# Optimization experiments

Measured on AMD Instinct MI355X. Metric: run time of the kernel, lower is better.

## Reference

```python
import jax, jax.numpy as jnp
import numpy as np

N, E, D, G = 50000, 600000, 128, 64
EPS = 1e-5


def prelu(x, a):
    return jnp.where(x >= 0, x, a * x)


def degree_norms(edge_src, edge_dst):
    ones = jnp.ones((E,), jnp.float32)
    deg_out = jax.ops.segment_sum(ones, edge_src, num_segments=N)
    deg_in = jax.ops.segment_sum(ones, edge_dst, num_segments=N)
    norm_src = jnp.where(deg_out > 0, jax.lax.rsqrt(jnp.maximum(deg_out, 1.0)), 0.0)
    norm_dst = jnp.where(deg_in > 0, jax.lax.rsqrt(jnp.maximum(deg_in, 1.0)), 0.0)
    return norm_src, norm_dst


def graph_conv(x, W, b, alpha, edge_src, edge_dst, norm_src, norm_dst):
    # DGL GraphConv norm='both': D_out^{-1/2} on src, aggregate, D_in^{-1/2} on dst, then linear
    xs = x * norm_src[:, None]
    agg = jax.ops.segment_sum(xs[edge_src], edge_dst, num_segments=N)
    agg = agg * norm_dst[:, None]
    h = agg @ W + b
    return prelu(h, alpha)


def batch_norm(h, gamma, beta):
    mean = jnp.mean(h, axis=0)
    var = jnp.mean(jnp.square(h - mean), axis=0)
    return (h - mean) * jax.lax.rsqrt(var + EPS) * gamma + beta


def setup_inputs() -> dict:
    key = jax.random.key(0)
    ks = jax.random.split(key, 8)
    inp = {
        "heat": jax.random.normal(ks[0], (N, D), jnp.float32),
        "edge_src": jax.random.randint(ks[1], (E,), 0, N, jnp.int32),
        "edge_dst": jax.random.randint(ks[2], (E,), 0, N, jnp.int32),
        "graph_ids": jnp.sort(jax.random.randint(ks[3], (N,), 0, G, jnp.int32)),
    }
    for i in range(2):
        kw = jax.random.fold_in(ks[4], i)
        inp[f"W{i}"] = jax.random.normal(kw, (D, D), jnp.float32) * (1.0 / np.sqrt(D))
        inp[f"b{i}"] = jnp.zeros((D,), jnp.float32)
        inp[f"ac{i}"] = jnp.float32(0.25)  # conv PReLU alpha
        inp[f"g{i}"] = jnp.ones((D,), jnp.float32)
        inp[f"be{i}"] = jnp.zeros((D,), jnp.float32)
        inp[f"aa{i}"] = jnp.float32(0.25)  # outer PReLU alpha
    return inp


def reference(heat, edge_src, edge_dst, graph_ids,
              W0, b0, ac0, g0, be0, aa0,
              W1, b1, ac1, g1, be1, aa1):
    norm_src, norm_dst = degree_norms(edge_src, edge_dst)
    x = heat  # dropout in eval mode -> identity
    h = graph_conv(x, W0, b0, ac0, edge_src, edge_dst, norm_src, norm_dst)
    h = prelu(batch_norm(h, g0, be0), aa0)
    gh = jax.ops.segment_sum(h, graph_ids, num_segments=G)
    h = graph_conv(h, W1, b1, ac1, edge_src, edge_dst, norm_src, norm_dst)
    h = prelu(batch_norm(h, g1, be1), aa1)
    gh = gh + jax.ops.segment_sum(h, graph_ids, num_segments=G)
    return h, gh
```

## Files before the change

### kernel.cpp

```cpp
#include <hip/hip_runtime.h>
#include <hip/hip_fp8.h>

#define NN 50000
#define NE 600000
#define DD 128
#define GG 64
#define EPS 1e-5f
#define CAP 64
#define HB 60
#define ECHUNK 10000
#define HALF 25000
#define HWORDS 12500
#define ZROW 50000
#define NBUILD ((NE + 255) / 256)
#define NPB (NN * 16 / 256)

typedef unsigned short u16;
typedef unsigned int u32;
typedef unsigned char u8;
typedef u16 u16x8 __attribute__((ext_vector_type(8)));
typedef u8 u8x16 __attribute__((ext_vector_type(16)));
typedef u8 u8x8 __attribute__((ext_vector_type(8)));
typedef short bf16x8 __attribute__((ext_vector_type(8)));
typedef float f32x4 __attribute__((ext_vector_type(4)));

__device__ __forceinline__ float bf2f(u16 v) {
    return __uint_as_float(((u32)v) << 16);
}
__device__ __forceinline__ u16 f2bf(float f) {
    u32 u = __float_as_uint(f);
    u += 0x7fff + ((u >> 16) & 1);
    return (u16)(u >> 16);
}
__device__ __forceinline__ float f8tof(u8 b) {
    __hip_fp8_e4m3 v;
    v.__x = b;
    return (float)v;
}
__device__ __forceinline__ u8 ftof8(float f) {
    return __hip_fp8_e4m3(f).__x;
}

__global__ void k_wprep(const float* __restrict__ W0, const float* __restrict__ W1,
                        u16* __restrict__ wtb, int* __restrict__ cnt_in,
                        float* __restrict__ stats , float* __restrict__ gh,
                        u8* __restrict__ xsb) {
    int k = threadIdx.x;
    int c = blockIdx.x;
    int lay = blockIdx.y;
    const float* W = lay ? W1 : W0;
    wtb[lay * DD * DD + c * DD + k] = f2bf(W[k * DD + c]);

    int gtid = (blockIdx.y * gridDim.x + blockIdx.x) * DD + threadIdx.x;
    for (int i = gtid; i < NN; i += 32768) cnt_in[i] = 0;
    if (gtid < 4 * DD) stats[gtid] = 0.f;
    if (gtid < GG * DD) gh[gtid] = 0.f;
    if (gtid < 16) {
        u8x8 z = {0, 0, 0, 0, 0, 0, 0, 0};
        *(u8x8*)(xsb + (size_t)ZROW * DD + gtid * 8) = z;
    }
}

__global__ __launch_bounds__(256) void k_prep(
        const int* __restrict__ src, const int* __restrict__ dst,
        u32* __restrict__ partials, int* __restrict__ cnt_in, u16* __restrict__ csr) {
    __shared__ u32 hc[HWORDS];
    int blk = blockIdx.x;
    int t = threadIdx.x;
    if (blk >= 2 * HB) {
        int e = (blk - 2 * HB) * 256 + t;
        if (e < NE) {
            int d = dst[e];
            int pos = atomicAdd(&cnt_in[d], 1);
            if (pos < CAP) csr[(size_t)d * CAP + pos] = (u16)src[e];
        }
        return;
    }
    int b = blk % HB, p = blk / HB;
    for (int i = t; i < HWORDS; i += 256) hc[i] = 0;
    __syncthreads();
    int lo = p * HALF;
    int e0 = b * ECHUNK;
    for (int e = e0 + t; e < e0 + ECHUNK; e += 256) {
        int s = src[e] - lo;
        if ((u32)s < (u32)HALF) atomicAdd(&hc[s >> 1], 1u << ((s & 1) << 4));
    }
    __syncthreads();
    u32* outp = partials + (size_t)(p * HB + b) * HWORDS;
    for (int i = t; i < HWORDS; i += 256) outp[i] = hc[i];
}

__global__ void k_hist_reduce(const u32* __restrict__ partials, const int* __restrict__ cnt_in,
                              float* __restrict__ norm_src, float* __restrict__ norm_dst) {
    int j = blockIdx.x * 256 + threadIdx.x;
    int p = blockIdx.y;
    if (j < HWORDS) {
        u32 s = 0;
#pragma unroll 4
        for (int b = 0; b < HB; ++b) s += partials[(size_t)(p * HB + b) * HWORDS + j];
        int n0 = p * HALF + 2 * j;
        u32 c0 = s & 0xffffu, c1 = s >> 16;
        norm_src[n0]     = c0 ? rsqrtf((float)c0) : 0.f;
        norm_src[n0 + 1] = c1 ? rsqrtf((float)c1) : 0.f;
        int d0 = cnt_in[n0], d1 = cnt_in[n0 + 1];
        norm_dst[n0]     = d0 > 0 ? rsqrtf((float)d0) : 0.f;
        norm_dst[n0 + 1] = d1 > 0 ? rsqrtf((float)d1) : 0.f;
    }
}

__global__ void k_scale_rows(const float* __restrict__ norm_src, const float* __restrict__ x,
                             u8* __restrict__ xsb) {
    int idx = blockIdx.x * 256 + threadIdx.x;
    int row = idx >> 4;
    int c8 = (idx & 15) << 3;
    float ns = norm_src[row];
    const float4* xp = (const float4*)(x + (size_t)row * DD + c8);
    float4 a = xp[0], b = xp[1];
    u8x8 o;
    o[0] = ftof8(a.x * ns); o[1] = ftof8(a.y * ns); o[2] = ftof8(a.z * ns); o[3] = ftof8(a.w * ns);
    o[4] = ftof8(b.x * ns); o[5] = ftof8(b.y * ns); o[6] = ftof8(b.z * ns); o[7] = ftof8(b.w * ns);
    *(u8x8*)(xsb + (size_t)row * DD + c8) = o;
}

#define LOADF8(v, ii)                                                    \
    u8x16 v##0 = *(const u8x16*)(xcol + (size_t)(ii)[0] * DD);           \
    u8x16 v##1 = *(const u8x16*)(xcol + (size_t)(ii)[1] * DD);           \
    u8x16 v##2 = *(const u8x16*)(xcol + (size_t)(ii)[2] * DD);           \
    u8x16 v##3 = *(const u8x16*)(xcol + (size_t)(ii)[3] * DD);           \
    u8x16 v##4 = *(const u8x16*)(xcol + (size_t)(ii)[4] * DD);           \
    u8x16 v##5 = *(const u8x16*)(xcol + (size_t)(ii)[5] * DD);           \
    u8x16 v##6 = *(const u8x16*)(xcol + (size_t)(ii)[6] * DD);           \
    u8x16 v##7 = *(const u8x16*)(xcol + (size_t)(ii)[7] * DD);

#define ACCF8(acc, v)                                                    \
    _Pragma("unroll")                                                    \
    for (int j = 0; j < 16; ++j) {                                       \
        float a01 = f8tof(v##0[j]) + f8tof(v##1[j]);                     \
        float a23 = f8tof(v##2[j]) + f8tof(v##3[j]);                     \
        float a45 = f8tof(v##4[j]) + f8tof(v##5[j]);                     \
        float a67 = f8tof(v##6[j]) + f8tof(v##7[j]);                     \
        acc[j] += (a01 + a23) + (a45 + a67);                             \
    }

__global__ __launch_bounds__(256) void k_gg(
        const u8* __restrict__ xsb, const int* __restrict__ cnt_in,
        const u16* __restrict__ csr, const float* __restrict__ norm_dst,
        const u16* __restrict__ wtb, const float* __restrict__ bias,
        const float* __restrict__ ac, u16* __restrict__ hpreb,
        float* __restrict__ sums, float* __restrict__ sumsq) {
    __shared__ u16 sAg[4][16][DD + 8];
    __shared__ float sStat[2][4][DD];
    int t = threadIdx.x;
    int w = t >> 6;
    int l = t & 63;
    int rb = blockIdx.x * 64 + w * 16;
    bool wvalid = (rb < NN);
    int cl8 = l & 7;
    int rw = l >> 3;
    const u8* xcol = xsb + cl8 * 16;

    if (wvalid) {
#pragma unroll
        for (int gp = 0; gp < 2; ++gp) {
            int r = rb + gp * 8 + rw;
            int cnt = min(cnt_in[r], CAP);
            const u16* ce = csr + (size_t)r * CAP;
            float acc[16];
#pragma unroll
            for (int j = 0; j < 16; ++j) acc[j] = 0.f;
            int e = 0;
            for (; e + 8 <= cnt; e += 8) {
                u16x8 ii = *(const u16x8*)(ce + e);
                LOADF8(va, ii)
                ACCF8(acc, va)
            }
            if (e < cnt) {
                u16x8 ii = *(const u16x8*)(ce + e);
                int jj[8];
#pragma unroll
                for (int j = 0; j < 8; ++j) jj[j] = (e + j < cnt) ? (int)ii[j] : ZROW;
                LOADF8(vm, jj)
                ACCF8(acc, vm)
            }
            float nd = norm_dst[r];
            u16x8 o0, o1;
#pragma unroll
            for (int j = 0; j < 8; ++j) {
                o0[j] = f2bf(acc[j] * nd);
                o1[j] = f2bf(acc[8 + j] * nd);
            }
            *(u16x8*)&sAg[w][gp * 8 + rw][cl8 * 16] = o0;
            *(u16x8*)&sAg[w][gp * 8 + rw][cl8 * 16 + 8] = o1;
        }
    }
    __syncthreads();

    int lr = l & 15;
    int kg = l >> 4;
    float alpha = ac[0];

    bf16x8 afrag[4];
    if (wvalid) {
        const u16* abase = &sAg[w][lr][kg * 8];
        afrag[0] = *(const bf16x8*)(abase);
        afrag[1] = *(const bf16x8*)(abase + 32);
        afrag[2] = *(const bf16x8*)(abase + 64);
        afrag[3] = *(const bf16x8*)(abase + 96);
    }

#pragma unroll
    for (int ct = 0; ct < 8; ++ct) {
        int c = ct * 16;
        float sS = 0.f, sQ = 0.f;
        if (wvalid) {
            const u16* bbase = wtb + (size_t)(c + lr) * DD + kg * 8;
            bf16x8 b0 = *(const bf16x8*)(bbase);
            bf16x8 b1 = *(const bf16x8*)(bbase + 32);
            bf16x8 b2 = *(const bf16x8*)(bbase + 64);
            bf16x8 b3 = *(const bf16x8*)(bbase + 96);
            float bv = bias[c + lr];
            f32x4 acc = {bv, bv, bv, bv};
            acc = __builtin_amdgcn_mfma_f32_16x16x32_bf16(afrag[0], b0, acc, 0, 0, 0);
            acc = __builtin_amdgcn_mfma_f32_16x16x32_bf16(afrag[1], b1, acc, 0, 0, 0);
            acc = __builtin_amdgcn_mfma_f32_16x16x32_bf16(afrag[2], b2, acc, 0, 0, 0);
            acc = __builtin_amdgcn_mfma_f32_16x16x32_bf16(afrag[3], b3, acc, 0, 0, 0);
#pragma unroll
            for (int j = 0; j < 4; ++j) {
                float h = acc[j];
                h = h >= 0.f ? h : alpha * h;
                u16 hb = f2bf(h);
                float hq = bf2f(hb);
                int grow = rb + kg * 4 + j;
                hpreb[(size_t)grow * DD + c + lr] = hb;
                sS += hq;
                sQ += hq * hq;
            }
        }
        sS += __shfl_xor(sS, 16); sS += __shfl_xor(sS, 32);
        sQ += __shfl_xor(sQ, 16); sQ += __shfl_xor(sQ, 32);
        if (kg == 0) {
            sStat[0][w][c + lr] = sS;
            sStat[1][w][c + lr] = sQ;
        }
    }
    __syncthreads();
    if (t < DD) {
        float s = sStat[0][0][t] + sStat[0][1][t] + sStat[0][2][t] + sStat[0][3][t];
        atomicAdd(&sums[t], s);
    } else if (t < 2 * DD) {
        int c = t - DD;
        float q = sStat[1][0][c] + sStat[1][1][c] + sStat[1][2][c] + sStat[1][3][c];
        atomicAdd(&sumsq[c], q);
    }
}

__global__ __launch_bounds__(256) void k_post(
        const u16* __restrict__ hpreb,
        const float* __restrict__ sums, const float* __restrict__ sumsq,
        const float* __restrict__ gamma, const float* __restrict__ beta,
        const float* __restrict__ aa, const float* __restrict__ nsrc,
        float* __restrict__ h_out, u8* __restrict__ xs_next, int writeXs,
        const int* __restrict__ gids, float* __restrict__ gh) {
    __shared__ float sc[DD], sh[DD];
    __shared__ float red[2][DD];
    int t = threadIdx.x;
    if (t < DD) {
        float mean = sums[t] * (1.0f / NN);
        float var = sumsq[t] * (1.0f / NN) - mean * mean;
        float inv = rsqrtf(var + EPS);
        float s = inv * gamma[t];
        sc[t] = s;
        sh[t] = beta[t] - mean * s;
    }
    __syncthreads();
    float a = aa[0];
    int blk = blockIdx.x;

    if (blk < NPB) {
        int idx = blk * 256 + t;
        int row = idx >> 4;
        int c8 = (idx & 15) << 3;
        u16x8 hv = *(const u16x8*)(hpreb + (size_t)idx * 8);
        float v[8];
#pragma unroll
        for (int j = 0; j < 8; ++j) v[j] = bf2f(hv[j]) * sc[c8 + j] + sh[c8 + j];
#pragma unroll
        for (int j = 0; j < 8; ++j) v[j] = v[j] >= 0.f ? v[j] : a * v[j];
        float4* op = (float4*)(h_out + (size_t)idx * 8);
        op[0] = make_float4(v[0], v[1], v[2], v[3]);
        op[1] = make_float4(v[4], v[5], v[6], v[7]);
        if (writeXs) {
            float ns = nsrc[row];
            u8x8 o;
#pragma unroll
            for (int j = 0; j < 8; ++j) o[j] = ftof8(v[j] * ns);
            *(u8x8*)(xs_next + (size_t)row * DD + c8) = o;
        }
        return;
    }

    int sb = blk - NPB;
    int g = sb & (GG - 1);
    int slice = sb >> 6;
    int lo, hi;
    {
        int l = 0, r = NN;
        while (l < r) { int m = (l + r) >> 1; if (gids[m] < g) l = m + 1; else r = m; }
        lo = l;
        r = NN;
        while (l < r) { int m = (l + r) >> 1; if (gids[m] < g + 1) l = m + 1; else r = m; }
        hi = l;
    }
    int cnt = hi - lo;
    int chunk = (cnt + 7) >> 3;
    int s0 = lo + slice * chunk;
    int s1 = min(s0 + chunk, hi);
    int c = t & 127;
    int half = t >> 7;
    float s = 0.f;
    for (int row = s0 + half; row < s1; row += 2) {
        float v = bf2f(hpreb[(size_t)row * DD + c]) * sc[c] + sh[c];
        v = v >= 0.f ? v : a * v;
        s += v;
    }
    red[half][c] = s;
    __syncthreads();
    if (t < DD)
        atomicAdd(&gh[g * DD + t], red[0][t] + red[1][t]);
}

extern "C" void kernel_launch(void* const* d_in, const int* in_sizes, int n_in,
                              void* d_out, int out_size, void* d_ws, size_t ws_size,
                              hipStream_t stream) {
    const float* heat = (const float*)d_in[0];
    const int* esrc = (const int*)d_in[1];
    const int* edst = (const int*)d_in[2];
    const int* gids = (const int*)d_in[3];
    const float* Wp[2]  = {(const float*)d_in[4],  (const float*)d_in[10]};
    const float* bp[2]  = {(const float*)d_in[5],  (const float*)d_in[11]};
    const float* acp[2] = {(const float*)d_in[6],  (const float*)d_in[12]};
    const float* gp[2]  = {(const float*)d_in[7],  (const float*)d_in[13]};
    const float* bep[2] = {(const float*)d_in[8],  (const float*)d_in[14]};
    const float* aap[2] = {(const float*)d_in[9],  (const float*)d_in[15]};

    float* out = (float*)d_out;
    float* h_out = out;
    float* gh = out + (size_t)NN * DD;

    char* wsp = (char*)d_ws;
    int* cnt_in_i   = (int*)wsp;              wsp += NN * sizeof(int);
    float* norm_src = (float*)wsp;            wsp += NN * sizeof(float);
    float* norm_dst = (float*)wsp;            wsp += NN * sizeof(float);
    float* stats    = (float*)wsp;            wsp += 4 * DD * sizeof(float);
    u16* wtb        = (u16*)wsp;              wsp += 2 * DD * DD * sizeof(u16);
    u8* xsb         = (u8*)wsp;               wsp += (size_t)(NN + 1) * DD;
    u16* hpreb      = (u16*)wsp;              wsp += (size_t)NN * DD * sizeof(u16);
    u16* csr        = (u16*)wsp;              wsp += (size_t)NN * CAP * sizeof(u16);
    u32* partials   = (u32*)wsp;              wsp += (size_t)2 * HB * HWORDS * sizeof(u32);

    dim3 gwp(DD, 2);
    k_wprep<<<gwp, DD, 0, stream>>>(Wp[0], Wp[1], wtb, cnt_in_i, stats, gh, xsb);
    k_prep<<<2 * HB + NBUILD, 256, 0, stream>>>(esrc, edst, partials, cnt_in_i, csr);
    dim3 gred((HWORDS + 255) / 256, 2);
    k_hist_reduce<<<gred, 256, 0, stream>>>(partials, cnt_in_i, norm_src, norm_dst);
    k_scale_rows<<<NN * 16 / 256, 256, 0, stream>>>(norm_src, heat, xsb);

    for (int layer = 0; layer < 2; ++layer) {
        float* sums_l  = stats + layer * 2 * DD;
        float* sumsq_l = sums_l + DD;
        k_gg<<<(NN + 63) / 64, 256, 0, stream>>>(xsb, cnt_in_i, csr, norm_dst,
                                                 wtb + layer * DD * DD, bp[layer], acp[layer],
                                                 hpreb, sums_l, sumsq_l);
        k_post<<<NPB + GG * 8, 256, 0, stream>>>(hpreb, sums_l, sumsq_l,
                                                 gp[layer], bep[layer], aap[layer],
                                                 norm_src, h_out, xsb, layer == 0 ? 1 : 0,
                                                 gids, gh);
    }
}
```

Baseline: 216.7 us.

## Fold prep kernels into fewer launches and skip layer-0 h_out write

Removes the separate weight-prep and histogram-reduce kernels. Weight transposition moves into extra blocks of k_prep, the src-degree reduction is fused into k_scale_rows with a warp shuffle, and norm_dst is computed inline in k_gg from cnt_in. Zeroing now uses hipMemsetAsync. k_post no longer writes the fp32 h_out in layer 0, since layer 1 overwrites it. This cuts launches and removes one full 25.6MB write, at the cost of the redundant partial reads spreading across more blocks.

```diff
diff --git a/kernel.cpp b/kernel.cpp
--- a/kernel.cpp
+++ b/kernel.cpp
@@ -13,6 +13,8 @@
 #define HWORDS 12500
 #define ZROW 50000
 #define NBUILD ((NE + 255) / 256)
+#define WB0 (2 * HB + NBUILD)
+#define NWTB 128
 #define NPB (NN * 16 / 256)
 
 typedef unsigned short u16;
@@ -41,32 +43,27 @@
     return __hip_fp8_e4m3(f).__x;
 }
 
-__global__ void k_wprep(const float* __restrict__ W0, const float* __restrict__ W1,
-                        u16* __restrict__ wtb, int* __restrict__ cnt_in,
-                        float* __restrict__ stats , float* __restrict__ gh,
-                        u8* __restrict__ xsb) {
-    int k = threadIdx.x;
-    int c = blockIdx.x;
-    int lay = blockIdx.y;
-    const float* W = lay ? W1 : W0;
-    wtb[lay * DD * DD + c * DD + k] = f2bf(W[k * DD + c]);
-
-    int gtid = (blockIdx.y * gridDim.x + blockIdx.x) * DD + threadIdx.x;
-    for (int i = gtid; i < NN; i += 32768) cnt_in[i] = 0;
-    if (gtid < 4 * DD) stats[gtid] = 0.f;
-    if (gtid < GG * DD) gh[gtid] = 0.f;
-    if (gtid < 16) {
-        u8x8 z = {0, 0, 0, 0, 0, 0, 0, 0};
-        *(u8x8*)(xsb + (size_t)ZROW * DD + gtid * 8) = z;
-    }
-}
-
 __global__ __launch_bounds__(256) void k_prep(
         const int* __restrict__ src, const int* __restrict__ dst,
-        u32* __restrict__ partials, int* __restrict__ cnt_in, u16* __restrict__ csr) {
+        u32* __restrict__ partials, int* __restrict__ cnt_in, u16* __restrict__ csr,
+        const float* __restrict__ W0, const float* __restrict__ W1,
+        u16* __restrict__ wtb, u8* __restrict__ xsb) {
     __shared__ u32 hc[HWORDS];
     int blk = blockIdx.x;
     int t = threadIdx.x;
+    if (blk >= WB0) {
+        int gt = (blk - WB0) * 256 + t;
+        int lay = gt >> 14;
+        int rem = gt & 16383;
+        int c = rem >> 7, k = rem & 127;
+        const float* W = lay ? W1 : W0;
+        wtb[lay * DD * DD + c * DD + k] = f2bf(W[k * DD + c]);
+        if (gt < 16) {
+            u8x8 z = {0, 0, 0, 0, 0, 0, 0, 0};
+            *(u8x8*)(xsb + (size_t)ZROW * DD + gt * 8) = z;
+        }
+        return;
+    }
     if (blk >= 2 * HB) {
         int e = (blk - 2 * HB) * 256 + t;
         if (e < NE) {
@@ -90,35 +87,44 @@
     for (int i = t; i < HWORDS; i += 256) outp[i] = hc[i];
 }
 
-__global__ void k_hist_reduce(const u32* __restrict__ partials, const int* __restrict__ cnt_in,
-                              float* __restrict__ norm_src, float* __restrict__ norm_dst) {
-    int j = blockIdx.x * 256 + threadIdx.x;
-    int p = blockIdx.y;
-    if (j < HWORDS) {
-        u32 s = 0;
-#pragma unroll 4
-        for (int b = 0; b < HB; ++b) s += partials[(size_t)(p * HB + b) * HWORDS + j];
-        int n0 = p * HALF + 2 * j;
-        u32 c0 = s & 0xffffu, c1 = s >> 16;
-        norm_src[n0]     = c0 ? rsqrtf((float)c0) : 0.f;
-        norm_src[n0 + 1] = c1 ? rsqrtf((float)c1) : 0.f;
-        int d0 = cnt_in[n0], d1 = cnt_in[n0 + 1];
-        norm_dst[n0]     = d0 > 0 ? rsqrtf((float)d0) : 0.f;
-        norm_dst[n0 + 1] = d1 > 0 ? rsqrtf((float)d1) : 0.f;
-    }
-}
-
-__global__ void k_scale_rows(const float* __restrict__ norm_src, const float* __restrict__ x,
-                             u8* __restrict__ xsb) {
-    int idx = blockIdx.x * 256 + threadIdx.x;
+__global__ __launch_bounds__(256) void k_scale_rows(
+        const u32* __restrict__ partials, const float* __restrict__ x,
+        float* __restrict__ norm_src, u8* __restrict__ xsb) {
+    __shared__ float snorm[16];
+    int blk = blockIdx.x;
+    int t = threadIdx.x;
+    int rb = blk * 16;
+    int s = t >> 5, c = t & 31;
+    int rA = rb + 2 * s;
+    int p = rA / HALF;
+    int j = (rA - p * HALF) >> 1;
+    u32 sum = 0;
+    for (int b = c; b < HB; b += 32)
+        sum += partials[(size_t)(p * HB + b) * HWORDS + j];
+    sum += __shfl_xor((int)sum, 1);
+    sum += __shfl_xor((int)sum, 2);
+    sum += __shfl_xor((int)sum, 4);
+    sum += __shfl_xor((int)sum, 8);
+    sum += __shfl_xor((int)sum, 16);
+    if (c == 0) {
+        u32 c0 = sum & 0xffffu, c1 = sum >> 16;
+        float n0 = c0 ? rsqrtf((float)c0) : 0.f;
+        float n1 = c1 ? rsqrtf((float)c1) : 0.f;
+        snorm[2 * s] = n0;
+        snorm[2 * s + 1] = n1;
+        norm_src[rA] = n0;
+        norm_src[rA + 1] = n1;
+    }
+    __syncthreads();
+    int idx = blk * 256 + t;
     int row = idx >> 4;
     int c8 = (idx & 15) << 3;
-    float ns = norm_src[row];
+    float ns = snorm[t >> 4];
     const float4* xp = (const float4*)(x + (size_t)row * DD + c8);
-    float4 a = xp[0], b = xp[1];
+    float4 a = xp[0], b2 = xp[1];
     u8x8 o;
     o[0] = ftof8(a.x * ns); o[1] = ftof8(a.y * ns); o[2] = ftof8(a.z * ns); o[3] = ftof8(a.w * ns);
-    o[4] = ftof8(b.x * ns); o[5] = ftof8(b.y * ns); o[6] = ftof8(b.z * ns); o[7] = ftof8(b.w * ns);
+    o[4] = ftof8(b2.x * ns); o[5] = ftof8(b2.y * ns); o[6] = ftof8(b2.z * ns); o[7] = ftof8(b2.w * ns);
     *(u8x8*)(xsb + (size_t)row * DD + c8) = o;
 }
 
@@ -144,7 +150,7 @@
 
 __global__ __launch_bounds__(256) void k_gg(
         const u8* __restrict__ xsb, const int* __restrict__ cnt_in,
-        const u16* __restrict__ csr, const float* __restrict__ norm_dst,
+        const u16* __restrict__ csr,
         const u16* __restrict__ wtb, const float* __restrict__ bias,
         const float* __restrict__ ac, u16* __restrict__ hpreb,
         float* __restrict__ sums, float* __restrict__ sumsq) {
@@ -163,7 +169,8 @@
 #pragma unroll
         for (int gp = 0; gp < 2; ++gp) {
             int r = rb + gp * 8 + rw;
-            int cnt = min(cnt_in[r], CAP);
+            int craw = cnt_in[r];
+            int cnt = min(craw, CAP);
             const u16* ce = csr + (size_t)r * CAP;
             float acc[16];
 #pragma unroll
@@ -182,7 +189,7 @@
                 LOADF8(vm, jj)
                 ACCF8(acc, vm)
             }
-            float nd = norm_dst[r];
+            float nd = craw > 0 ? rsqrtf((float)craw) : 0.f;
             u16x8 o0, o1;
 #pragma unroll
             for (int j = 0; j < 8; ++j) {
@@ -259,7 +266,7 @@
         const float* __restrict__ sums, const float* __restrict__ sumsq,
         const float* __restrict__ gamma, const float* __restrict__ beta,
         const float* __restrict__ aa, const float* __restrict__ nsrc,
-        float* __restrict__ h_out, u8* __restrict__ xs_next, int writeXs,
+        float* __restrict__ h_out, u8* __restrict__ xs_next, int lastLayer,
         const int* __restrict__ gids, float* __restrict__ gh) {
     __shared__ float sc[DD], sh[DD];
     __shared__ float red[2][DD];
@@ -286,10 +293,11 @@
         for (int j = 0; j < 8; ++j) v[j] = bf2f(hv[j]) * sc[c8 + j] + sh[c8 + j];
 #pragma unroll
         for (int j = 0; j < 8; ++j) v[j] = v[j] >= 0.f ? v[j] : a * v[j];
-        float4* op = (float4*)(h_out + (size_t)idx * 8);
-        op[0] = make_float4(v[0], v[1], v[2], v[3]);
-        op[1] = make_float4(v[4], v[5], v[6], v[7]);
-        if (writeXs) {
+        if (lastLayer) {
+            float4* op = (float4*)(h_out + (size_t)idx * 8);
+            op[0] = make_float4(v[0], v[1], v[2], v[3]);
+            op[1] = make_float4(v[4], v[5], v[6], v[7]);
+        } else {
             float ns = nsrc[row];
             u8x8 o;
 #pragma unroll
@@ -349,31 +357,30 @@
 
     char* wsp = (char*)d_ws;
     int* cnt_in_i   = (int*)wsp;              wsp += NN * sizeof(int);
+    float* stats    = (float*)wsp;            wsp += 4 * DD * sizeof(float);
     float* norm_src = (float*)wsp;            wsp += NN * sizeof(float);
-    float* norm_dst = (float*)wsp;            wsp += NN * sizeof(float);
-    float* stats    = (float*)wsp;            wsp += 4 * DD * sizeof(float);
     u16* wtb        = (u16*)wsp;              wsp += 2 * DD * DD * sizeof(u16);
     u8* xsb         = (u8*)wsp;               wsp += (size_t)(NN + 1) * DD;
     u16* hpreb      = (u16*)wsp;              wsp += (size_t)NN * DD * sizeof(u16);
     u16* csr        = (u16*)wsp;              wsp += (size_t)NN * CAP * sizeof(u16);
     u32* partials   = (u32*)wsp;              wsp += (size_t)2 * HB * HWORDS * sizeof(u32);
 
-    dim3 gwp(DD, 2);
-    k_wprep<<<gwp, DD, 0, stream>>>(Wp[0], Wp[1], wtb, cnt_in_i, stats, gh, xsb);
-    k_prep<<<2 * HB + NBUILD, 256, 0, stream>>>(esrc, edst, partials, cnt_in_i, csr);
-    dim3 gred((HWORDS + 255) / 256, 2);
-    k_hist_reduce<<<gred, 256, 0, stream>>>(partials, cnt_in_i, norm_src, norm_dst);
-    k_scale_rows<<<NN * 16 / 256, 256, 0, stream>>>(norm_src, heat, xsb);
+    hipMemsetAsync(cnt_in_i, 0, NN * sizeof(int) + 4 * DD * sizeof(float), stream);
+    hipMemsetAsync(gh, 0, GG * DD * sizeof(float), stream);
+
+    k_prep<<<WB0 + NWTB, 256, 0, stream>>>(esrc, edst, partials, cnt_in_i, csr,
+                                           Wp[0], Wp[1], wtb, xsb);
+    k_scale_rows<<<NPB, 256, 0, stream>>>(partials, heat, norm_src, xsb);
 
     for (int layer = 0; layer < 2; ++layer) {
         float* sums_l  = stats + layer * 2 * DD;
         float* sumsq_l = sums_l + DD;
-        k_gg<<<(NN + 63) / 64, 256, 0, stream>>>(xsb, cnt_in_i, csr, norm_dst,
+        k_gg<<<(NN + 63) / 64, 256, 0, stream>>>(xsb, cnt_in_i, csr,
                                                  wtb + layer * DD * DD, bp[layer], acp[layer],
                                                  hpreb, sums_l, sumsq_l);
         k_post<<<NPB + GG * 8, 256, 0, stream>>>(hpreb, sums_l, sumsq_l,
                                                  gp[layer], bep[layer], aap[layer],
-                                                 norm_src, h_out, xsb, layer == 0 ? 1 : 0,
+                                                 norm_src, h_out, xsb, layer == 1 ? 1 : 0,
                                                  gids, gh);
     }
 }
```

Result: faster. 210.8 us (-2.7%).
